# Performance work log

Measured on AMD Instinct MI355X. Metric: run time of the kernel, lower is better.

The kernel has to match this reference:

```python
import jax, jax.numpy as jnp
import numpy as np

NEG_INF = -1e30

def _pool_unpool(x, k):
    # x: [B, C, H, W]. Non-overlapping max pool with window k (floor-mode,
    # matching torch MaxPool2d default), then MaxUnpool: scatter the pooled max
    # back to its argmax location within each window, zeros elsewhere.
    B, C, H, W = x.shape
    Hc, Wc = (H // k) * k, (W // k) * k  # cropped region covered by windows
    xc = x[:, :, :Hc, :Wc]
    # reshape into windows: [B, C, H/k, k, W/k, k] -> [B, C, H/k, W/k, k*k]
    xw = xc.reshape(B, C, Hc // k, k, Wc // k, k).transpose(0, 1, 2, 4, 3, 5)
    xw = xw.reshape(B, C, Hc // k, Wc // k, k * k)
    mx = jnp.max(xw, axis=-1, keepdims=True)
    am = jnp.argmax(xw, axis=-1)  # first max index, matches torch tie-breaking
    onehot = (jnp.arange(k * k) == am[..., None])
    yw = jnp.where(onehot, mx, jnp.zeros_like(mx))
    yc = yw.reshape(B, C, Hc // k, Wc // k, k, k).transpose(0, 1, 2, 4, 3, 5)
    yc = yc.reshape(B, C, Hc, Wc)
    # output_size=size in torch unpool -> pad uncovered border with zeros
    return jnp.pad(yc, ((0, 0), (0, 0), (0, H - Hc), (0, W - Wc)))

def setup_inputs() -> dict:
    key = jax.random.key(0)
    x = jax.random.uniform(key, (16, 1, 1080, 1920), dtype=jnp.float32)
    return {"x": x}

def reference(x):
    k = 3
    x = _pool_unpool(x, k)
    x = _pool_unpool(x, k + 2)
    x = _pool_unpool(x, k + 3)
    return x
```

## Files before the change

### kernel.cpp

```cpp
#include <hip/hip_runtime.h>


#define IMG_H 1080
#define IMG_W 1920
#define TILE_H 30
#define TILE_W 240
#define NTHREADS 256

template <int K>
__device__ __forceinline__ void nms_stage(float (*tile)[TILE_W], int t) {
    constexpr int NWR = TILE_H / K;
    constexpr int NWC = TILE_W / K;
    for (int w = t; w < NWR * NWC; w += NTHREADS) {
        const int wr = w / NWC;
        const int wc = w - wr * NWC;
        const int r0 = wr * K;
        const int c0 = wc * K;
        float mx = -1.0f;
        int am = 0;
#pragma unroll
        for (int r = 0; r < K; ++r)
#pragma unroll
            for (int c = 0; c < K; ++c) {
                const float v = tile[r0 + r][c0 + c];
                if (v > mx) { mx = v; am = r * K + c; }
            }
#pragma unroll
        for (int r = 0; r < K; ++r)
#pragma unroll
            for (int c = 0; c < K; ++c)
                tile[r0 + r][c0 + c] = (r * K + c == am) ? mx : 0.0f;
    }
    __syncthreads();
}

__global__ __launch_bounds__(NTHREADS) void pooling_nms_kernel(
    const float* __restrict__ x, float* __restrict__ out) {
    __shared__ float tile[TILE_H][TILE_W];

    const int t = threadIdx.x;
    const int col0 = blockIdx.x * TILE_W;
    const int row0 = blockIdx.y * TILE_H;
    const size_t base = (size_t)blockIdx.z * (IMG_H * (size_t)IMG_W) +
                        (size_t)row0 * IMG_W + col0;
    const float* src = x + base;
    float* dst = out + base;

    constexpr int VPR = TILE_W / 4;
    constexpr int NV = TILE_H * VPR;
    for (int i = t; i < NV; i += NTHREADS) {
        const int r = i / VPR;
        const int c4 = i - r * VPR;
        const float4 v =
            *reinterpret_cast<const float4*>(src + (size_t)r * IMG_W + c4 * 4);
        *reinterpret_cast<float4*>(&tile[r][c4 * 4]) = v;
    }
    __syncthreads();

    nms_stage<3>(tile, t);
    nms_stage<5>(tile, t);
    nms_stage<6>(tile, t);

    for (int i = t; i < NV; i += NTHREADS) {
        const int r = i / VPR;
        const int c4 = i - r * VPR;
        *reinterpret_cast<float4*>(dst + (size_t)r * IMG_W + c4 * 4) =
            *reinterpret_cast<const float4*>(&tile[r][c4 * 4]);
    }
}

extern "C" void kernel_launch(void* const* d_in, const int* in_sizes, int n_in,
                              void* d_out, int out_size, void* d_ws, size_t ws_size,
                              hipStream_t stream) {
    const float* x = (const float*)d_in[0];
    float* out = (float*)d_out;
    dim3 grid(IMG_W / TILE_W, IMG_H / TILE_H, 16);
    pooling_nms_kernel<<<grid, NTHREADS, 0, stream>>>(x, out);
}
```

Before: 238.9 us.

## Use persistent blocks with double-buffered async global-to-LDS strip prefetch

```diff
diff --git a/kernel.cpp b/kernel.cpp
--- a/kernel.cpp
+++ b/kernel.cpp
@@ -1,4 +1,5 @@
 #include <hip/hip_runtime.h>
+#include <stdint.h>
 
 
 #define IMG_H 1080
@@ -6,6 +7,18 @@
 #define TILE_H 30
 #define TILE_W 240
 #define NTHREADS 256
+#define V4PR (TILE_W / 4)
+#define NV4 (TILE_H * V4PR)
+
+#define NSX (IMG_W / TILE_W)
+#define NSY (IMG_H / TILE_H)
+#define NB 16
+#define NSTRIPS (NSX * NSY * NB)
+#define NBLOCKS 512
+#define SPB (NSTRIPS / NBLOCKS)
+
+#define GPTR(p) ((const __attribute__((address_space(1))) void*)(p))
+#define LPTR(p) ((__attribute__((address_space(3))) void*)(p))
 
 template <int K>
 __device__ __forceinline__ void nms_stage(float (*tile)[TILE_W], int t) {
@@ -31,41 +44,66 @@
             for (int c = 0; c < K; ++c)
                 tile[r0 + r][c0 + c] = (r * K + c == am) ? mx : 0.0f;
     }
-    __syncthreads();
 }
 
 __global__ __launch_bounds__(NTHREADS) void pooling_nms_kernel(
     const float* __restrict__ x, float* __restrict__ out) {
-    __shared__ float tile[TILE_H][TILE_W];
+    __shared__ float tile[2][TILE_H][TILE_W];
 
     const int t = threadIdx.x;
-    const int col0 = blockIdx.x * TILE_W;
-    const int row0 = blockIdx.y * TILE_H;
-    const size_t base = (size_t)blockIdx.z * (IMG_H * (size_t)IMG_W) +
-                        (size_t)row0 * IMG_W + col0;
-    const float* src = x + base;
-    float* dst = out + base;
+    const int s0 = blockIdx.x * SPB;
 
-    constexpr int VPR = TILE_W / 4;
-    constexpr int NV = TILE_H * VPR;
-    for (int i = t; i < NV; i += NTHREADS) {
-        const int r = i / VPR;
-        const int c4 = i - r * VPR;
-        const float4 v =
-            *reinterpret_cast<const float4*>(src + (size_t)r * IMG_W + c4 * 4);
-        *reinterpret_cast<float4*>(&tile[r][c4 * 4]) = v;
-    }
-    __syncthreads();
+    const int r_t = t / V4PR;
+    const int c4_t = t - r_t * V4PR;
 
-    nms_stage<3>(tile, t);
-    nms_stage<5>(tile, t);
-    nms_stage<6>(tile, t);
+    auto strip_base = [&](int s) -> size_t {
+        const int xs = s % NSX;
+        const int rem = s / NSX;
+        const int ys = rem % NSY;
+        const int z = rem / NSY;
+        return (size_t)z * (IMG_H * (size_t)IMG_W) +
+               (size_t)(ys * TILE_H) * IMG_W + (size_t)xs * TILE_W;
+    };
 
-    for (int i = t; i < NV; i += NTHREADS) {
-        const int r = i / VPR;
-        const int c4 = i - r * VPR;
-        *reinterpret_cast<float4*>(dst + (size_t)r * IMG_W + c4 * 4) =
-            *reinterpret_cast<const float4*>(&tile[r][c4 * 4]);
+    auto prefetch = [&](int s, int buf) {
+        const float* src = x + strip_base(s);
+        int r = r_t, c4 = c4_t;
+        for (int v = t; v < NV4; v += NTHREADS) {
+            __builtin_amdgcn_global_load_lds(
+                GPTR(src + (size_t)r * IMG_W + c4 * 4),
+                LPTR((char*)&tile[buf][0][0] + (size_t)v * 16), 16, 0, 0);
+            r += 4; c4 += 16;
+            if (c4 >= V4PR) { c4 -= V4PR; r += 1; }
+        }
+    };
+
+    auto store_strip = [&](int s, int buf) {
+        float* dst = out + strip_base(s);
+        int r = r_t, c4 = c4_t;
+        for (int v = t; v < NV4; v += NTHREADS) {
+            *reinterpret_cast<float4*>(dst + (size_t)r * IMG_W + c4 * 4) =
+                *reinterpret_cast<const float4*>(&tile[buf][r][c4 * 4]);
+            r += 4; c4 += 16;
+            if (c4 >= V4PR) { c4 -= V4PR; r += 1; }
+        }
+    };
+
+    prefetch(s0, 0);
+    asm volatile("s_waitcnt vmcnt(0)\n\ts_barrier" ::: "memory");
+
+    for (int i = 0; i < SPB; ++i) {
+        const int buf = i & 1;
+        if (i + 1 < SPB) prefetch(s0 + i + 1, buf ^ 1);
+
+        nms_stage<3>(tile[buf], t);
+        asm volatile("s_waitcnt lgkmcnt(0)\n\ts_barrier" ::: "memory");
+        nms_stage<5>(tile[buf], t);
+        asm volatile("s_waitcnt lgkmcnt(0)\n\ts_barrier" ::: "memory");
+        nms_stage<6>(tile[buf], t);
+        asm volatile("s_waitcnt lgkmcnt(0)\n\ts_barrier" ::: "memory");
+
+        store_strip(s0 + i, buf);
+        asm volatile("s_waitcnt vmcnt(7) lgkmcnt(0)\n\ts_barrier" ::: "memory");
     }
 }
 
@@ -74,6 +112,5 @@
                               hipStream_t stream) {
     const float* x = (const float*)d_in[0];
     float* out = (float*)d_out;
-    dim3 grid(IMG_W / TILE_W, IMG_H / TILE_H, 16);
-    pooling_nms_kernel<<<grid, NTHREADS, 0, stream>>>(x, out);
+    pooling_nms_kernel<<<dim3(NBLOCKS), NTHREADS, 0, stream>>>(x, out);
 }
```

Measured after the change: 249.6 us. 4.5% more time.
